# Optimization experiments

Measured on AMD Instinct MI355X. Metric: run time of the kernel, lower is better.

Reference implementation:

```python
import jax, jax.numpy as jnp
import numpy as np

E, T, D = 100000, 400000, 128
LN_EPS = 1e-5


def setup_inputs() -> dict:
    key = jax.random.key(0)
    k1, k2, k3 = jax.random.split(key, 3)
    f_edge = jax.random.normal(k1, (E, D), dtype=jnp.float32)
    W = jax.random.normal(k2, (3 * D, D), dtype=jnp.float32) / np.sqrt(3 * D)
    b = jnp.zeros((D,), dtype=jnp.float32)
    gamma = jnp.ones((D,), dtype=jnp.float32)
    beta = jnp.zeros((D,), dtype=jnp.float32)
    triangle = jax.random.randint(k3, (T, 3), 0, E, dtype=jnp.int64)
    return {"f_edge": f_edge, "W": W, "b": b, "gamma": gamma, "beta": beta,
            "triangle": triangle}


def reference(f_edge, W, b, gamma, beta, triangle):
    # f_edge [E, D], triangle [T, 3] -> gather to [T, 3, D], flatten to [T, 3D]
    t = triangle.shape[0]
    e, d = f_edge.shape
    f_tri = f_edge[triangle].reshape(t, 3 * d)
    # Linear(3D -> D) + exact GELU (torch nn.GELU default is erf-based)
    h = jax.nn.gelu(f_tri @ W + b, approximate=False)  # [T, D]
    # scatter_mean over destination edge index triangle[:, 2], dim_size=E
    dst = triangle[:, 2]
    seg_sum = jax.ops.segment_sum(h, dst, num_segments=e)            # [E, D]
    cnt = jax.ops.segment_sum(jnp.ones((t,), h.dtype), dst, num_segments=e)
    mean = seg_sum / jnp.maximum(cnt, 1.0)[:, None]
    # dropout is identity in eval mode; LayerNorm over last dim
    mu = jnp.mean(mean, axis=-1, keepdims=True)
    var = jnp.mean(jnp.square(mean - mu), axis=-1, keepdims=True)
    return (mean - mu) / jnp.sqrt(var + LN_EPS) * gamma + beta
```

## Files before the change

### kernel.cpp

```cpp
#include <hip/hip_runtime.h>
#include <hip/hip_bf16.h>

typedef __attribute__((ext_vector_type(8))) short short8;
typedef __attribute__((ext_vector_type(4))) float floatx4;
typedef __attribute__((ext_vector_type(4))) unsigned int uintx4;

__device__ __forceinline__ float gelu_fast(float x)
{
    float u = 0.7978845608f * x * (1.0f + 0.044715f * x * x);
    float e = __builtin_amdgcn_exp2f(2.885390082f * u);
    return x - x * __builtin_amdgcn_rcpf(e + 1.0f);
}

__global__ __launch_bounds__(256)
void prep(const float* __restrict__ Wg, uintx4* __restrict__ wq,
          const int* __restrict__ tri, int* __restrict__ cnt,
          int* __restrict__ slot, int T)
{
    int g = blockIdx.x * 256 + threadIdx.x;
    if (g < T) {
        int i2 = tri[g * 3 + 2];
        slot[g] = atomicAdd(&cnt[i2], 1);
    } else {
        int i = g - T;
        if (i < 6144) {
            int frag = i >> 6, lane = i & 63;
            int ko = frag >> 3, nt = frag & 7;
            int col = lane & 15, quad = lane >> 4;
            unsigned short tmp[8] __attribute__((aligned(16)));
#pragma unroll
            for (int j = 0; j < 8; ++j) {
                __hip_bfloat16 b =
                    __float2bfloat16(Wg[(ko * 32 + quad * 8 + j) * 128 + nt * 16 + col]);
                tmp[j] = *(unsigned short*)&b;
            }
            wq[i] = *(const uintx4*)tmp;
        }
    }
}

__device__ __forceinline__ int wave_incl_scan(int v, int lane)
{
#pragma unroll
    for (int o = 1; o < 64; o <<= 1) {
        int u = __shfl_up(v, o);
        if (lane >= o) v += u;
    }
    return v;
}

__global__ __launch_bounds__(1024)
void scan_blk(const int* __restrict__ in, int* __restrict__ outExcl,
              int* __restrict__ partial, int n)
{
    __shared__ int ws[16];
    int t = threadIdx.x;
    int g = blockIdx.x * 1024 + t;
    int lane = t & 63, wv = t >> 6;
    int v = (g < n) ? in[g] : 0;
    int sc = wave_incl_scan(v, lane);
    if (lane == 63) ws[wv] = sc;
    __syncthreads();
    if (wv == 0) {
        int b = (lane < 16) ? ws[lane] : 0;
        int bs = wave_incl_scan(b, lane);
        if (lane < 16) ws[lane] = bs;
    }
    __syncthreads();
    int off = wv ? ws[wv - 1] : 0;
    if (g < n) outExcl[g] = off + sc - v;
    if (partial && t == 0) partial[blockIdx.x] = ws[15];
}

__global__ __launch_bounds__(256)
void scatter(const int* __restrict__ tri, const int* __restrict__ slot,
             const int* __restrict__ excl, const int* __restrict__ pscan,
             int2* __restrict__ srec, int T)
{
    int g = blockIdx.x * 256 + threadIdx.x;
    if (g >= T) return;
    int i0 = tri[g * 3 + 0];
    int i1 = tri[g * 3 + 1];
    int i2 = tri[g * 3 + 2];
    int pos = excl[i2] + pscan[i2 >> 10] + slot[g];
    srec[pos] = make_int2(i0 << 8, i1 << 8);
}

__global__ __launch_bounds__(1024, 1)
void edge_gemm(const float* __restrict__ fe_f, const uintx4* __restrict__ wq,
               unsigned short* __restrict__ G, int E)
{
    __shared__ uintx4 ldsW[6144];

    const int tid  = threadIdx.x;
    const int wv   = tid >> 6;
    const int lane = tid & 63;
    const int col  = lane & 15;
    const int quad = lane >> 4;
    const int ntiles = (E + 15) >> 4;

    for (int i = tid; i < 6144; i += 1024) ldsW[i] = wq[i];
    __syncthreads();

#pragma unroll 1
    for (int tile = blockIdx.x * 16 + wv; tile < ntiles; tile += gridDim.x * 16) {
        int row_a = tile * 16 + col;
        if (row_a >= E) row_a = E - 1;
        const float* arow = fe_f + (size_t)row_a * 128 + quad * 8;

        floatx4 f[8];
#pragma unroll
        for (int l = 0; l < 8; ++l)
            f[l] = *(const floatx4*)(arow + (l >> 1) * 32 + (l & 1) * 4);

        short8 a[4];
#pragma unroll
        for (int ko = 0; ko < 4; ++ko) {
            unsigned short tmp[8] __attribute__((aligned(16)));
#pragma unroll
            for (int j = 0; j < 8; ++j) {
                __hip_bfloat16 b = __float2bfloat16(f[ko * 2 + (j >> 2)][j & 3]);
                tmp[j] = *(unsigned short*)&b;
            }
            a[ko] = *(const short8*)tmp;
        }

#pragma unroll 1
        for (int r = 0; r < 3; ++r) {
            floatx4 acc[8];
#pragma unroll
            for (int nt = 0; nt < 8; ++nt) acc[nt] = (floatx4)0.0f;

#pragma unroll
            for (int ko = 0; ko < 4; ++ko) {
#pragma unroll
                for (int nt = 0; nt < 8; ++nt) {
                    short8 bf = *(const short8*)&ldsW[r * 2048 + (ko * 8 + nt) * 64 + lane];
                    acc[nt] = __builtin_amdgcn_mfma_f32_16x16x32_bf16(a[ko], bf, acc[nt], 0, 0, 0);
                }
            }

            unsigned short* Gr = G + (size_t)r * E * 128;
#pragma unroll
            for (int rr = 0; rr < 4; ++rr) {
                int row = tile * 16 + quad * 4 + rr;
                if (row < E) {
                    unsigned short pk[8] __attribute__((aligned(16)));
#pragma unroll
                    for (int nt = 0; nt < 8; ++nt) {
                        __hip_bfloat16 hb = __float2bfloat16(acc[nt][rr]);
                        pk[nt] = *(unsigned short*)&hb;
                    }
                    *(uintx4*)(Gr + (size_t)row * 128 + col * 8) = *(const uintx4*)pk;
                }
            }
        }
    }
}

__global__ __launch_bounds__(256)
void mean_ln(const unsigned short* __restrict__ G, const int* __restrict__ cnt,
             const int* __restrict__ excl, const int* __restrict__ pscan,
             const int2* __restrict__ srec, const float* __restrict__ bias,
             const float* __restrict__ gamma, const float* __restrict__ beta,
             float* __restrict__ out, int E)
{
    int lane = threadIdx.x & 63;
    int row  = blockIdx.x * 4 + (threadIdx.x >> 6);
    if (row >= E) return;
    int col = lane & 15, q = lane >> 4;
    int boff = (col << 4) + (q << 2);
    const char* g0 = (const char*)G + boff;
    const char* g1 = g0 + (size_t)E * 256;
    const char* g2 = g1 + (size_t)E * 256;
    int j0 = q * 32 + col, j1 = j0 + 16;

    unsigned int w2 = *(const unsigned int*)(g2 + (size_t)row * 256);
    float base0 = __uint_as_float(w2 << 16) + bias[j0];
    float base1 = __uint_as_float(w2 & 0xffff0000u) + bias[j1];

    int s = excl[row] + pscan[row >> 10];
    int c = cnt[row];

    float x0 = 0.0f, x1 = 0.0f;
    for (int p = 0; p < c; p += 64) {
        int nav = min(64, c - p);
        int2 rr = srec[s + p + (lane < nav ? lane : 0)];
        for (int k = 0; k < nav; ++k) {
            int o0 = __shfl(rr.x, k);
            int o1 = __shfl(rr.y, k);
            unsigned int w0 = *(const unsigned int*)(g0 + (size_t)(unsigned)o0);
            unsigned int w1 = *(const unsigned int*)(g1 + (size_t)(unsigned)o1);
            float s0 = __uint_as_float(w0 << 16) + __uint_as_float(w1 << 16) + base0;
            float s1 = __uint_as_float(w0 & 0xffff0000u)
                     + __uint_as_float(w1 & 0xffff0000u) + base1;
            x0 += gelu_fast(s0);
            x1 += gelu_fast(s1);
        }
    }

    float inv = 1.0f / fmaxf((float)c, 1.0f);
    float m0 = x0 * inv, m1 = x1 * inv;
    float sm = m0 + m1;
#pragma unroll
    for (int o = 32; o > 0; o >>= 1) sm += __shfl_xor(sm, o);
    float mu = sm * (1.0f / 128.0f);
    float d0 = m0 - mu, d1 = m1 - mu;
    float v = d0 * d0 + d1 * d1;
#pragma unroll
    for (int o = 32; o > 0; o >>= 1) v += __shfl_xor(v, o);
    float rstd = rsqrtf(v * (1.0f / 128.0f) + 1e-5f);
    out[(size_t)row * 128 + j0] = d0 * rstd * gamma[j0] + beta[j0];
    out[(size_t)row * 128 + j1] = d1 * rstd * gamma[j1] + beta[j1];
}

extern "C" void kernel_launch(void* const* d_in, const int* in_sizes, int n_in,
                              void* d_out, int out_size, void* d_ws, size_t ws_size,
                              hipStream_t stream)
{
    const float* fe_f  = (const float*)d_in[0];
    const float* Wg    = (const float*)d_in[1];
    const float* bias  = (const float*)d_in[2];
    const float* gamma = (const float*)d_in[3];
    const float* beta  = (const float*)d_in[4];
    const int*   tri   = (const int*)d_in[5];

    int E = in_sizes[0] / 128;
    int T = in_sizes[5] / 3;

    unsigned short* G = (unsigned short*)d_ws;
    int2* srec = (int2*)((char*)d_ws + (size_t)3 * E * 256);
    uintx4* wq = (uintx4*)(srec + T);
    int* slot = (int*)(wq + 6144);
    int* cnt  = slot + T;
    int* excl = cnt + E;
    int* partial = excl + E;
    int* pscan = partial + 1024;

    hipMemsetAsync(cnt, 0, (size_t)E * sizeof(int), stream);

    int total = T + 6144;
    prep<<<(total + 255) / 256, 256, 0, stream>>>(Wg, wq, tri, cnt, slot, T);

    int NB = (E + 1023) / 1024;
    scan_blk<<<NB, 1024, 0, stream>>>(cnt, excl, partial, E);
    scan_blk<<<1, 1024, 0, stream>>>(partial, pscan, nullptr, NB);

    scatter<<<(T + 255) / 256, 256, 0, stream>>>(tri, slot, excl, pscan, srec, T);

    edge_gemm<<<256, 1024, 0, stream>>>(fe_f, wq, G, E);

    mean_ln<<<(E + 3) / 4, 256, 0, stream>>>(G, cnt, excl, pscan, srec,
                                             bias, gamma, beta, (float*)d_out, E);
}
```

Baseline: 223.4 us.

## Fuse preprocessing into one cooperative kernel and batch gathers in mean_ln

Replaces the memset plus four small preprocessing launches (count, two-level scan, scatter) with one cooperative kernel that separates phases with grid-wide syncs, and precomputes per-row (start, count) pairs. The mean/LayerNorm kernel now reads one packed rowinfo entry and issues eight gathers before the GELU math, so more loads are in flight at once. This removes launch gaps and intermediate round trips, at the cost of grid-sync overhead and more registers for the batched loads.

```diff
diff --git a/kernel.cpp b/kernel.cpp
--- a/kernel.cpp
+++ b/kernel.cpp
@@ -1,5 +1,8 @@
 #include <hip/hip_runtime.h>
 #include <hip/hip_bf16.h>
+#include <hip/hip_cooperative_groups.h>
+
+namespace cg = cooperative_groups;
 
 typedef __attribute__((ext_vector_type(8))) short short8;
 typedef __attribute__((ext_vector_type(4))) float floatx4;
@@ -12,33 +15,6 @@
     return x - x * __builtin_amdgcn_rcpf(e + 1.0f);
 }
 
-__global__ __launch_bounds__(256)
-void prep(const float* __restrict__ Wg, uintx4* __restrict__ wq,
-          const int* __restrict__ tri, int* __restrict__ cnt,
-          int* __restrict__ slot, int T)
-{
-    int g = blockIdx.x * 256 + threadIdx.x;
-    if (g < T) {
-        int i2 = tri[g * 3 + 2];
-        slot[g] = atomicAdd(&cnt[i2], 1);
-    } else {
-        int i = g - T;
-        if (i < 6144) {
-            int frag = i >> 6, lane = i & 63;
-            int ko = frag >> 3, nt = frag & 7;
-            int col = lane & 15, quad = lane >> 4;
-            unsigned short tmp[8] __attribute__((aligned(16)));
-#pragma unroll
-            for (int j = 0; j < 8; ++j) {
-                __hip_bfloat16 b =
-                    __float2bfloat16(Wg[(ko * 32 + quad * 8 + j) * 128 + nt * 16 + col]);
-                tmp[j] = *(unsigned short*)&b;
-            }
-            wq[i] = *(const uintx4*)tmp;
-        }
-    }
-}
-
 __device__ __forceinline__ int wave_incl_scan(int v, int lane)
 {
 #pragma unroll
@@ -50,40 +26,87 @@
 }
 
 __global__ __launch_bounds__(1024)
-void scan_blk(const int* __restrict__ in, int* __restrict__ outExcl,
-              int* __restrict__ partial, int n)
+void prep_all(const float* __restrict__ Wg, uintx4* __restrict__ wq,
+              const int* __restrict__ tri, int* __restrict__ cnt,
+              int* __restrict__ slot, int* __restrict__ excl,
+              int* __restrict__ partial, int* __restrict__ pscan,
+              int2* __restrict__ srec, int2* __restrict__ rowinfo,
+              int E, int T)
 {
     __shared__ int ws[16];
-    int t = threadIdx.x;
-    int g = blockIdx.x * 1024 + t;
-    int lane = t & 63, wv = t >> 6;
-    int v = (g < n) ? in[g] : 0;
-    int sc = wave_incl_scan(v, lane);
-    if (lane == 63) ws[wv] = sc;
-    __syncthreads();
-    if (wv == 0) {
-        int b = (lane < 16) ? ws[lane] : 0;
-        int bs = wave_incl_scan(b, lane);
-        if (lane < 16) ws[lane] = bs;
-    }
-    __syncthreads();
-    int off = wv ? ws[wv - 1] : 0;
-    if (g < n) outExcl[g] = off + sc - v;
-    if (partial && t == 0) partial[blockIdx.x] = ws[15];
-}
-
-__global__ __launch_bounds__(256)
-void scatter(const int* __restrict__ tri, const int* __restrict__ slot,
-             const int* __restrict__ excl, const int* __restrict__ pscan,
-             int2* __restrict__ srec, int T)
-{
-    int g = blockIdx.x * 256 + threadIdx.x;
-    if (g >= T) return;
-    int i0 = tri[g * 3 + 0];
-    int i1 = tri[g * 3 + 1];
-    int i2 = tri[g * 3 + 2];
-    int pos = excl[i2] + pscan[i2 >> 10] + slot[g];
-    srec[pos] = make_int2(i0 << 8, i1 << 8);
+    cg::grid_group grid = cg::this_grid();
+    const int tid  = threadIdx.x;
+    const int g    = blockIdx.x * 1024 + tid;
+    const int nthr = gridDim.x * 1024;
+    const int lane = tid & 63, wv = tid >> 6;
+
+    for (int i = g; i < E; i += nthr) cnt[i] = 0;
+    for (int i = g; i < 6144; i += nthr) {
+        int frag = i >> 6, l = i & 63;
+        int ko = frag >> 3, nt = frag & 7;
+        int col = l & 15, quad = l >> 4;
+        unsigned short tmp[8] __attribute__((aligned(16)));
+#pragma unroll
+        for (int j = 0; j < 8; ++j) {
+            __hip_bfloat16 b =
+                __float2bfloat16(Wg[(ko * 32 + quad * 8 + j) * 128 + nt * 16 + col]);
+            tmp[j] = *(unsigned short*)&b;
+        }
+        wq[i] = *(const uintx4*)tmp;
+    }
+    grid.sync();
+
+    for (int i = g; i < T; i += nthr) {
+        int i2 = tri[i * 3 + 2];
+        slot[i] = atomicAdd(&cnt[i2], 1);
+    }
+    grid.sync();
+
+    int nchunks = (E + 1023) >> 10;
+    for (int ch = blockIdx.x; ch < nchunks; ch += gridDim.x) {
+        int e = ch * 1024 + tid;
+        int v = (e < E) ? cnt[e] : 0;
+        int sc = wave_incl_scan(v, lane);
+        if (lane == 63) ws[wv] = sc;
+        __syncthreads();
+        if (wv == 0) {
+            int b = (lane < 16) ? ws[lane] : 0;
+            int bs = wave_incl_scan(b, lane);
+            if (lane < 16) ws[lane] = bs;
+        }
+        __syncthreads();
+        int off = wv ? ws[wv - 1] : 0;
+        if (e < E) excl[e] = off + sc - v;
+        if (tid == 0) partial[ch] = ws[15];
+        __syncthreads();
+    }
+    grid.sync();
+
+    if (blockIdx.x == 0) {
+        int v = (tid < nchunks) ? partial[tid] : 0;
+        int sc = wave_incl_scan(v, lane);
+        if (lane == 63) ws[wv] = sc;
+        __syncthreads();
+        if (wv == 0) {
+            int b = (lane < 16) ? ws[lane] : 0;
+            int bs = wave_incl_scan(b, lane);
+            if (lane < 16) ws[lane] = bs;
+        }
+        __syncthreads();
+        int off = wv ? ws[wv - 1] : 0;
+        if (tid < nchunks) pscan[tid] = off + sc - v;
+    }
+    grid.sync();
+
+    for (int i = g; i < T; i += nthr) {
+        int i0 = tri[i * 3 + 0];
+        int i1 = tri[i * 3 + 1];
+        int i2 = tri[i * 3 + 2];
+        int pos = excl[i2] + pscan[i2 >> 10] + slot[i];
+        srec[pos] = make_int2(i0 << 8, i1 << 8);
+    }
+    for (int i = g; i < E; i += nthr)
+        rowinfo[i] = make_int2(excl[i] + pscan[i >> 10], cnt[i]);
 }
 
 __global__ __launch_bounds__(1024, 1)
@@ -159,8 +182,7 @@
 }
 
 __global__ __launch_bounds__(256)
-void mean_ln(const unsigned short* __restrict__ G, const int* __restrict__ cnt,
-             const int* __restrict__ excl, const int* __restrict__ pscan,
+void mean_ln(const unsigned short* __restrict__ G, const int2* __restrict__ rowinfo,
              const int2* __restrict__ srec, const float* __restrict__ bias,
              const float* __restrict__ gamma, const float* __restrict__ beta,
              float* __restrict__ out, int E)
@@ -175,27 +197,39 @@
     const char* g2 = g1 + (size_t)E * 256;
     int j0 = q * 32 + col, j1 = j0 + 16;
 
+    int2 ri = rowinfo[row];
+    int s = ri.x, c = ri.y;
+
     unsigned int w2 = *(const unsigned int*)(g2 + (size_t)row * 256);
     float base0 = __uint_as_float(w2 << 16) + bias[j0];
     float base1 = __uint_as_float(w2 & 0xffff0000u) + bias[j1];
 
-    int s = excl[row] + pscan[row >> 10];
-    int c = cnt[row];
-
     float x0 = 0.0f, x1 = 0.0f;
-    for (int p = 0; p < c; p += 64) {
-        int nav = min(64, c - p);
-        int2 rr = srec[s + p + (lane < nav ? lane : 0)];
-        for (int k = 0; k < nav; ++k) {
-            int o0 = __shfl(rr.x, k);
-            int o1 = __shfl(rr.y, k);
-            unsigned int w0 = *(const unsigned int*)(g0 + (size_t)(unsigned)o0);
-            unsigned int w1 = *(const unsigned int*)(g1 + (size_t)(unsigned)o1);
-            float s0 = __uint_as_float(w0 << 16) + __uint_as_float(w1 << 16) + base0;
-            float s1 = __uint_as_float(w0 & 0xffff0000u)
-                     + __uint_as_float(w1 & 0xffff0000u) + base1;
-            x0 += gelu_fast(s0);
-            x1 += gelu_fast(s1);
+    for (int p0 = 0; p0 < c; p0 += 64) {
+        int nav = min(64, c - p0);
+        int2 rr = srec[s + p0 + (lane < nav ? lane : 0)];
+        for (int p = 0; p < nav; p += 8) {
+            int n8 = min(8, nav - p);
+            unsigned int w0[8], w1[8];
+#pragma unroll
+            for (int j = 0; j < 8; ++j) {
+                int kk = p + (j < n8 ? j : 0);
+                int o0 = __shfl(rr.x, kk);
+                int o1 = __shfl(rr.y, kk);
+                w0[j] = *(const unsigned int*)(g0 + (size_t)(unsigned)o0);
+                w1[j] = *(const unsigned int*)(g1 + (size_t)(unsigned)o1);
+            }
+#pragma unroll
+            for (int j = 0; j < 8; ++j) {
+                if (j < n8) {
+                    float s0 = __uint_as_float(w0[j] << 16)
+                             + __uint_as_float(w1[j] << 16) + base0;
+                    float s1 = __uint_as_float(w0[j] & 0xffff0000u)
+                             + __uint_as_float(w1[j] & 0xffff0000u) + base1;
+                    x0 += gelu_fast(s0);
+                    x1 += gelu_fast(s1);
+                }
+            }
         }
     }
 
@@ -236,20 +270,16 @@
     int* excl = cnt + E;
     int* partial = excl + E;
     int* pscan = partial + 1024;
-
-    hipMemsetAsync(cnt, 0, (size_t)E * sizeof(int), stream);
-
-    int total = T + 6144;
-    prep<<<(total + 255) / 256, 256, 0, stream>>>(Wg, wq, tri, cnt, slot, T);
-
-    int NB = (E + 1023) / 1024;
-    scan_blk<<<NB, 1024, 0, stream>>>(cnt, excl, partial, E);
-    scan_blk<<<1, 1024, 0, stream>>>(partial, pscan, nullptr, NB);
-
-    scatter<<<(T + 255) / 256, 256, 0, stream>>>(tri, slot, excl, pscan, srec, T);
+    int2* rowinfo = (int2*)(pscan + 1024);
+
+    void* cargs[] = { (void*)&Wg, (void*)&wq, (void*)&tri, (void*)&cnt,
+                      (void*)&slot, (void*)&excl, (void*)&partial, (void*)&pscan,
+                      (void*)&srec, (void*)&rowinfo, (void*)&E, (void*)&T };
+    hipLaunchCooperativeKernel((const void*)prep_all, dim3(256), dim3(1024),
+                               cargs, 0, stream);
 
     edge_gemm<<<256, 1024, 0, stream>>>(fe_f, wq, G, E);
 
-    mean_ln<<<(E + 3) / 4, 256, 0, stream>>>(G, cnt, excl, pscan, srec,
-                                             bias, gamma, beta, (float*)d_out, E);
-}
+    mean_ln<<<(E + 3) / 4, 256, 0, stream>>>(G, rowinfo, srec, bias, gamma, beta,
+                                             (float*)d_out, E);
+}
```

Measured after the change: 384.9 us. 72.3% more time.
